# Kernel tuning notes

Measured on AMD Instinct MI355X. Metric: run time of the kernel, lower is better.

The kernel has to match this reference:

```python
import jax, jax.numpy as jnp
import numpy as np

N = 50000      # nodes
E = 1600000    # edges (avg degree 32)
F = 11         # atom_features
ED = 4         # edge_dim
L = 4          # num_layers
G = 500        # graphs in batch


def _lin(k, fi, fo, layers=True):
    s = 1.0 / np.sqrt(fi)
    kw, kb = jax.random.split(k)
    sw = (L, fi, fo) if layers else (fi, fo)
    sb = (L, fo) if layers else (fo,)
    return (jax.random.uniform(kw, sw, jnp.float32, -s, s),
            jax.random.uniform(kb, sb, jnp.float32, -s, s))


def setup_inputs() -> dict:
    key = jax.random.key(0)
    ks = jax.random.split(key, 16)
    inp = {}
    inp["h"] = jax.random.normal(ks[0], (N, F), jnp.float32)
    inp["pos"] = jax.random.normal(ks[1], (N, 3), jnp.float32)
    inp["edge_index"] = jax.random.randint(ks[2], (2, E), 0, N)
    inp["edge_attr"] = jax.random.normal(ks[3], (E, ED), jnp.float32)
    inp["batch"] = jnp.sort(jax.random.randint(ks[4], (N,), 0, G))
    # stacked per-layer linear params
    specs = [("W_msg1", "b_msg1", 2 * F + 1 + ED, F),
             ("W_msg2", "b_msg2", F, F),
             ("W_attn", "b_attn", F, 1),
             ("W_upd1", "b_upd1", 2 * F, F),
             ("W_upd2", "b_upd2", F, F),
             ("W_x1", "b_x1", 2 * F + 1 + ED, F),
             ("W_x2", "b_x2", F, F),
             ("W_x3", "b_x3", F, 1)]
    for i, (wn, bn, fi, fo) in enumerate(specs):
        w, b = _lin(ks[5 + i], fi, fo)
        inp[wn] = w
        inp[bn] = b
    w, b = _lin(ks[14], F, 1, layers=False)
    inp["W_pred"] = w
    inp["b_pred"] = b
    return inp


def reference(h, pos, edge_index, edge_attr, batch,
              W_msg1, b_msg1, W_msg2, b_msg2, W_attn, b_attn,
              W_upd1, b_upd1, W_upd2, b_upd2,
              W_x1, b_x1, W_x2, b_x2, W_x3, b_x3,
              W_pred, b_pred):
    src, dst = edge_index[0], edge_index[1]  # j (source), i (target)
    x = pos
    for l in range(L):
        h_i, h_j = h[dst], h[src]
        x_i, x_j = x[dst], x[src]
        d = jnp.linalg.norm(x_j - x_i, axis=-1, keepdims=True)  # [E,1]
        feat = jnp.concatenate([h_i, h_j, d * d, edge_attr], axis=-1)  # [E,27]
        m = jax.nn.silu(feat @ W_msg1[l] + b_msg1[l])
        m = jax.nn.silu(m @ W_msg2[l] + b_msg2[l])
        attn = jax.nn.sigmoid(m @ W_attn[l] + b_attn[l])
        msg_h = attn * m                                          # [E,F]
        phi = jax.nn.silu(feat @ W_x1[l] + b_x1[l])
        phi = jax.nn.silu(phi @ W_x2[l] + b_x2[l])
        phi = phi @ W_x3[l] + b_x3[l]                             # [E,1]
        msg_x = (x_i - x_j) / (d + 1.0) * phi                     # [E,3]
        agg_h = jax.ops.segment_sum(msg_h, dst, num_segments=N)
        agg_x = jax.ops.segment_sum(msg_x, dst, num_segments=N)
        upd = jax.nn.silu(jnp.concatenate([h, agg_h], axis=-1) @ W_upd1[l] + b_upd1[l])
        upd = upd @ W_upd2[l] + b_upd2[l]
        h = h + upd          # residual (h = h + h_upd in outer loop)
        x = x + agg_x        # out_x = x + agg_x
    # global mean pool over graphs, then linear head
    counts = jax.ops.segment_sum(jnp.ones((N, 1), h.dtype), batch, num_segments=G)
    h_graph = jax.ops.segment_sum(h, batch, num_segments=G) / jnp.maximum(counts, 1.0)
    return (h_graph @ W_pred + b_pred).reshape(-1)
```

## Files before the change

kernel.cpp:

```cpp
#include <hip/hip_runtime.h>

#define N_NODES 50000
#define N_EDGES 1600000
#define F 11
#define FEAT 27
#define NLAYERS 4
#define NGRAPH 500
#define NVALS 14
#define PRESTRIDE 24
#define NBLK 196

__device__ __forceinline__ float siluf(float v) { return v * (1.0f / (1.0f + __expf(-v))); }
__device__ __forceinline__ float sigmf(float v) { return 1.0f / (1.0f + __expf(-v)); }

__global__ __launch_bounds__(256) void hist_kernel(const int* __restrict__ dst,
                                                   int* __restrict__ deg) {
    int e = blockIdx.x * 256 + threadIdx.x;
    if (e < N_EDGES) atomicAdd(&deg[dst[e]], 1);
}

__global__ __launch_bounds__(256) void scan1_kernel(const int* __restrict__ deg,
                                                    int* __restrict__ part,
                                                    int* __restrict__ bsum) {
    int t = threadIdx.x;
    int i = blockIdx.x * 256 + t;
    int v = (i < N_NODES) ? deg[i] : 0;
    int lane = t & 63, wid = t >> 6;
    int s = v;
    #pragma unroll
    for (int off = 1; off < 64; off <<= 1) {
        int u = __shfl_up(s, off);
        if (lane >= off) s += u;
    }
    __shared__ int wsum[4];
    if (lane == 63) wsum[wid] = s;
    __syncthreads();
    int wpre = 0;
    #pragma unroll
    for (int w = 0; w < 4; ++w) if (w < wid) wpre += wsum[w];
    if (i < N_NODES) part[i] = s + wpre - v;
    if (t == 255) bsum[blockIdx.x] = s + wpre;
}

__global__ __launch_bounds__(256) void scan2_kernel(int* __restrict__ bsum) {
    int t = threadIdx.x;
    int v = (t < NBLK) ? bsum[t] : 0;
    int lane = t & 63, wid = t >> 6;
    int s = v;
    #pragma unroll
    for (int off = 1; off < 64; off <<= 1) {
        int u = __shfl_up(s, off);
        if (lane >= off) s += u;
    }
    __shared__ int wsum[4];
    if (lane == 63) wsum[wid] = s;
    __syncthreads();
    int wpre = 0;
    #pragma unroll
    for (int w = 0; w < 4; ++w) if (w < wid) wpre += wsum[w];
    if (t < NBLK) bsum[t] = s + wpre - v;
}

__global__ __launch_bounds__(256) void scan3_kernel(const int* __restrict__ part,
                                                    const int* __restrict__ bsum,
                                                    int* __restrict__ cursor) {
    int i = blockIdx.x * 256 + threadIdx.x;
    if (i < N_NODES) cursor[i] = part[i] + bsum[blockIdx.x];
}

__global__ __launch_bounds__(256) void scatter_kernel(
    const int* __restrict__ src, const int* __restrict__ dst,
    const float* __restrict__ eattr, int* __restrict__ cursor,
    int* __restrict__ ssrc, int* __restrict__ sdst, float4* __restrict__ sea) {
    int e = blockIdx.x * 256 + threadIdx.x;
    if (e >= N_EDGES) return;
    int d = dst[e];
    int pos = atomicAdd(&cursor[d], 1);
    ssrc[pos] = src[e];
    sdst[pos] = d;
    sea[pos] = reinterpret_cast<const float4*>(eattr)[e];
}

__global__ __launch_bounds__(256) void init_kernel(
    const float* __restrict__ h0, const float* __restrict__ pos,
    float* __restrict__ h, float* __restrict__ x,
    const float* __restrict__ Wm1, const float* __restrict__ bm1,
    const float* __restrict__ Wx1, const float* __restrict__ bx1,
    float* __restrict__ preA, float* __restrict__ preB)
{
    __shared__ float sM[2 * F * F], sX[2 * F * F], sbm[F], sbx[F];
    int t = threadIdx.x;
    for (int i2 = t; i2 < 2 * F * F; i2 += 256) { sM[i2] = Wm1[i2]; sX[i2] = Wx1[i2]; }
    if (t < F) { sbm[t] = bm1[t]; sbx[t] = bx1[t]; }
    __syncthreads();

    int n = blockIdx.x * 256 + t;
    if (n >= N_NODES) return;

    float hv[F];
    #pragma unroll
    for (int f2 = 0; f2 < F; ++f2) { hv[f2] = h0[n * F + f2]; h[n * F + f2] = hv[f2]; }
    #pragma unroll
    for (int k = 0; k < 3; ++k) x[n * 3 + k] = pos[n * 3 + k];

    float am[F], bm_[F], ax[F], bx_[F];
    #pragma unroll
    for (int o = 0; o < F; ++o) { am[o] = sbm[o]; ax[o] = sbx[o]; bm_[o] = 0.f; bx_[o] = 0.f; }
    #pragma unroll
    for (int fi = 0; fi < F; ++fi) {
        float v = hv[fi];
        #pragma unroll
        for (int o = 0; o < F; ++o) {
            am[o]  = fmaf(v, sM[fi * F + o], am[o]);
            bm_[o] = fmaf(v, sM[(F + fi) * F + o], bm_[o]);
            ax[o]  = fmaf(v, sX[fi * F + o], ax[o]);
            bx_[o] = fmaf(v, sX[(F + fi) * F + o], bx_[o]);
        }
    }
    #pragma unroll
    for (int o = 0; o < F; ++o) {
        preA[n * PRESTRIDE + o]     = am[o];
        preA[n * PRESTRIDE + F + o] = ax[o];
        preB[n * PRESTRIDE + o]     = bm_[o];
        preB[n * PRESTRIDE + F + o] = bx_[o];
    }
}

__global__ __launch_bounds__(256) void edge_kernel(
    const float* __restrict__ preA, const float* __restrict__ preB,
    const float* __restrict__ x,
    const int* __restrict__ ssrc, const int* __restrict__ sdst,
    const float4* __restrict__ sea,
    const float* __restrict__ Wm1,
    const float* __restrict__ Wm2, const float* __restrict__ bm2,
    const float* __restrict__ Wa,  const float* __restrict__ ba,
    const float* __restrict__ Wx1,
    const float* __restrict__ Wx2, const float* __restrict__ bx2,
    const float* __restrict__ Wx3, const float* __restrict__ bx3,
    float* __restrict__ agg_h, float* __restrict__ agg_x)
{
    __shared__ float sWm2[F * F], sWx2[F * F];
    __shared__ float sMd2[F], sMea[4 * F], sXd2[F], sXea[4 * F];
    __shared__ float sbm2[F], sWa[F], sbx2[F], sWx3[F];
    __shared__ float sba, sbx3;
    int t = threadIdx.x;
    for (int i2 = t; i2 < F * F; i2 += 256) { sWm2[i2] = Wm2[i2]; sWx2[i2] = Wx2[i2]; }
    if (t < F) {
        sMd2[t] = Wm1[22 * F + t]; sXd2[t] = Wx1[22 * F + t];
        sbm2[t] = bm2[t]; sWa[t] = Wa[t]; sbx2[t] = bx2[t]; sWx3[t] = Wx3[t];
    }
    if (t >= 64 && t < 64 + 4 * F) { int k = t - 64; sMea[k] = Wm1[23 * F + k]; sXea[k] = Wx1[23 * F + k]; }
    if (t == 0) { sba = ba[0]; sbx3 = bx3[0]; }
    __syncthreads();

    int e = blockIdx.x * 256 + t;
    if (e >= N_EDGES) return;

    int j = ssrc[e];
    int d = sdst[e];

    float pav[22], pbv[22];
    {
        const float4* pa4 = reinterpret_cast<const float4*>(preA + (size_t)d * PRESTRIDE);
        const float4* pb4 = reinterpret_cast<const float4*>(preB + (size_t)j * PRESTRIDE);
        #pragma unroll
        for (int q = 0; q < 5; ++q) {
            float4 va = pa4[q], vb = pb4[q];
            pav[4 * q + 0] = va.x; pav[4 * q + 1] = va.y; pav[4 * q + 2] = va.z; pav[4 * q + 3] = va.w;
            pbv[4 * q + 0] = vb.x; pbv[4 * q + 1] = vb.y; pbv[4 * q + 2] = vb.z; pbv[4 * q + 3] = vb.w;
        }
        float2 ta = *reinterpret_cast<const float2*>(preA + (size_t)d * PRESTRIDE + 20);
        float2 tb = *reinterpret_cast<const float2*>(preB + (size_t)j * PRESTRIDE + 20);
        pav[20] = ta.x; pav[21] = ta.y; pbv[20] = tb.x; pbv[21] = tb.y;
    }

    float xi0 = x[d * 3 + 0], xi1 = x[d * 3 + 1], xi2 = x[d * 3 + 2];
    float xj0 = x[j * 3 + 0], xj1 = x[j * 3 + 1], xj2 = x[j * 3 + 2];
    float dx = xj0 - xi0, dy = xj1 - xi1, dz = xj2 - xi2;
    float d2 = dx * dx + dy * dy + dz * dz;
    float4 ea = sea[e];

    float tm[F], tx[F];
    #pragma unroll
    for (int o = 0; o < F; ++o) {
        tm[o] = pav[o] + pbv[o];
        tx[o] = pav[F + o] + pbv[F + o];
    }
    #pragma unroll
    for (int o = 0; o < F; ++o) {
        tm[o] = fmaf(d2, sMd2[o], tm[o]);
        tx[o] = fmaf(d2, sXd2[o], tx[o]);
    }
    float eav[4] = {ea.x, ea.y, ea.z, ea.w};
    #pragma unroll
    for (int k = 0; k < 4; ++k) {
        float v = eav[k];
        #pragma unroll
        for (int o = 0; o < F; ++o) {
            tm[o] = fmaf(v, sMea[k * F + o], tm[o]);
            tx[o] = fmaf(v, sXea[k * F + o], tx[o]);
        }
    }
    #pragma unroll
    for (int o = 0; o < F; ++o) { tm[o] = siluf(tm[o]); tx[o] = siluf(tx[o]); }

    float m2[F], p2[F];
    #pragma unroll
    for (int o = 0; o < F; ++o) { m2[o] = sbm2[o]; p2[o] = sbx2[o]; }
    #pragma unroll
    for (int fi = 0; fi < F; ++fi) {
        float a = tm[fi], b = tx[fi];
        #pragma unroll
        for (int o = 0; o < F; ++o) {
            m2[o] = fmaf(a, sWm2[fi * F + o], m2[o]);
            p2[o] = fmaf(b, sWx2[fi * F + o], p2[o]);
        }
    }
    #pragma unroll
    for (int o = 0; o < F; ++o) { m2[o] = siluf(m2[o]); p2[o] = siluf(p2[o]); }

    float attn = sba, phi = sbx3;
    #pragma unroll
    for (int o = 0; o < F; ++o) {
        attn = fmaf(m2[o], sWa[o], attn);
        phi  = fmaf(p2[o], sWx3[o], phi);
    }
    attn = sigmf(attn);

    float dist = sqrtf(d2);
    float sc = phi / (dist + 1.0f);

    float vals[NVALS];
    #pragma unroll
    for (int o = 0; o < F; ++o) vals[o] = attn * m2[o];
    vals[F + 0] = (xi0 - xj0) * sc;
    vals[F + 1] = (xi1 - xj1) * sc;
    vals[F + 2] = (xi2 - xj2) * sc;

    int lane = t & 63;
    #pragma unroll
    for (int off = 1; off < 64; off <<= 1) {
        int du = __shfl_down(d, off);
        bool ok = (lane + off < 64) && (du == d);
        #pragma unroll
        for (int k = 0; k < NVALS; ++k) {
            float up = __shfl_down(vals[k], off);
            if (ok) vals[k] += up;
        }
    }
    int dprev = __shfl_up(d, 1);
    if (lane == 0 || dprev != d) {
        #pragma unroll
        for (int o = 0; o < F; ++o) unsafeAtomicAdd(&agg_h[d * F + o], vals[o]);
        unsafeAtomicAdd(&agg_x[d * 3 + 0], vals[F + 0]);
        unsafeAtomicAdd(&agg_x[d * 3 + 1], vals[F + 1]);
        unsafeAtomicAdd(&agg_x[d * 3 + 2], vals[F + 2]);
    }
}

__global__ __launch_bounds__(256) void node_kernel(
    float* __restrict__ h, float* __restrict__ x,
    const float* __restrict__ agg_h, const float* __restrict__ agg_x,
    const float* __restrict__ Wu1, const float* __restrict__ bu1,
    const float* __restrict__ Wu2, const float* __restrict__ bu2,
    const float* __restrict__ Wm1n, const float* __restrict__ bm1n,
    const float* __restrict__ Wx1n, const float* __restrict__ bx1n,
    float* __restrict__ preA, float* __restrict__ preB, int has_next)
{
    __shared__ float sWu1[2 * F * F], sWu2[F * F], sbu1[F], sbu2[F];
    __shared__ float sM[2 * F * F], sX[2 * F * F], sbm[F], sbx[F];
    int t = threadIdx.x;
    for (int i2 = t; i2 < 2 * F * F; i2 += 256) sWu1[i2] = Wu1[i2];
    for (int i2 = t; i2 < F * F; i2 += 256)     sWu2[i2] = Wu2[i2];
    if (t < F) { sbu1[t] = bu1[t]; sbu2[t] = bu2[t]; }
    if (has_next) {
        for (int i2 = t; i2 < 2 * F * F; i2 += 256) { sM[i2] = Wm1n[i2]; sX[i2] = Wx1n[i2]; }
        if (t < F) { sbm[t] = bm1n[t]; sbx[t] = bx1n[t]; }
    }
    __syncthreads();

    int n = blockIdx.x * 256 + t;
    if (n >= N_NODES) return;

    float in[2 * F];
    #pragma unroll
    for (int f2 = 0; f2 < F; ++f2) in[f2] = h[n * F + f2];
    #pragma unroll
    for (int f2 = 0; f2 < F; ++f2) in[F + f2] = agg_h[n * F + f2];

    float u[F];
    #pragma unroll
    for (int o = 0; o < F; ++o) u[o] = sbu1[o];
    #pragma unroll
    for (int fi = 0; fi < 2 * F; ++fi) {
        float fv = in[fi];
        #pragma unroll
        for (int o = 0; o < F; ++o) u[o] = fmaf(fv, sWu1[fi * F + o], u[o]);
    }
    #pragma unroll
    for (int o = 0; o < F; ++o) u[o] = siluf(u[o]);

    float hn[F];
    #pragma unroll
    for (int o = 0; o < F; ++o) hn[o] = in[o] + sbu2[o];
    #pragma unroll
    for (int fi = 0; fi < F; ++fi) {
        float fv = u[fi];
        #pragma unroll
        for (int o = 0; o < F; ++o) hn[o] = fmaf(fv, sWu2[fi * F + o], hn[o]);
    }

    #pragma unroll
    for (int f2 = 0; f2 < F; ++f2) h[n * F + f2] = hn[f2];
    #pragma unroll
    for (int k = 0; k < 3; ++k) x[n * 3 + k] += agg_x[n * 3 + k];

    if (has_next) {
        float am[F], bm_[F], ax[F], bx_[F];
        #pragma unroll
        for (int o = 0; o < F; ++o) { am[o] = sbm[o]; ax[o] = sbx[o]; bm_[o] = 0.f; bx_[o] = 0.f; }
        #pragma unroll
        for (int fi = 0; fi < F; ++fi) {
            float v = hn[fi];
            #pragma unroll
            for (int o = 0; o < F; ++o) {
                am[o]  = fmaf(v, sM[fi * F + o], am[o]);
                bm_[o] = fmaf(v, sM[(F + fi) * F + o], bm_[o]);
                ax[o]  = fmaf(v, sX[fi * F + o], ax[o]);
                bx_[o] = fmaf(v, sX[(F + fi) * F + o], bx_[o]);
            }
        }
        #pragma unroll
        for (int o = 0; o < F; ++o) {
            preA[n * PRESTRIDE + o]     = am[o];
            preA[n * PRESTRIDE + F + o] = ax[o];
            preB[n * PRESTRIDE + o]     = bm_[o];
            preB[n * PRESTRIDE + F + o] = bx_[o];
        }
    }
}

__global__ __launch_bounds__(256) void pool_kernel(
    const float* __restrict__ h, const int* __restrict__ batch,
    float* __restrict__ gsum, float* __restrict__ gcnt)
{
    int n = blockIdx.x * blockDim.x + threadIdx.x;
    int lane = threadIdx.x & 63;
    bool valid = (n < N_NODES);
    int g = valid ? batch[n] : -1;
    float vals[F + 1];
    #pragma unroll
    for (int f2 = 0; f2 < F; ++f2) vals[f2] = valid ? h[n * F + f2] : 0.0f;
    vals[F] = valid ? 1.0f : 0.0f;

    #pragma unroll
    for (int off = 1; off < 64; off <<= 1) {
        int gu = __shfl_down(g, off);
        bool ok = (lane + off < 64) && (gu == g);
        #pragma unroll
        for (int k = 0; k < F + 1; ++k) {
            float up = __shfl_down(vals[k], off);
            if (ok) vals[k] += up;
        }
    }
    int gprev = __shfl_up(g, 1);
    if (valid && (lane == 0 || gprev != g)) {
        #pragma unroll
        for (int f2 = 0; f2 < F; ++f2) unsafeAtomicAdd(&gsum[g * F + f2], vals[f2]);
        unsafeAtomicAdd(&gcnt[g], vals[F]);
    }
}

__global__ void head_kernel(const float* __restrict__ gsum, const float* __restrict__ gcnt,
                            const float* __restrict__ Wp, const float* __restrict__ bp,
                            float* __restrict__ out)
{
    int g = blockIdx.x * blockDim.x + threadIdx.x;
    if (g >= NGRAPH) return;
    float c = fmaxf(gcnt[g], 1.0f);
    float inv = 1.0f / c;
    float acc = bp[0];
    #pragma unroll
    for (int f2 = 0; f2 < F; ++f2) acc = fmaf(gsum[g * F + f2] * inv, Wp[f2], acc);
    out[g] = acc;
}

extern "C" void kernel_launch(void* const* d_in, const int* in_sizes, int n_in,
                              void* d_out, int out_size, void* d_ws, size_t ws_size,
                              hipStream_t stream)
{
    const float* h0    = (const float*)d_in[0];
    const float* pos   = (const float*)d_in[1];
    const int*   eidx  = (const int*)d_in[2];
    const float* eattr = (const float*)d_in[3];
    const int*   batch = (const int*)d_in[4];
    const float* Wm1 = (const float*)d_in[5];
    const float* bm1 = (const float*)d_in[6];
    const float* Wm2 = (const float*)d_in[7];
    const float* bm2 = (const float*)d_in[8];
    const float* Wa  = (const float*)d_in[9];
    const float* ba  = (const float*)d_in[10];
    const float* Wu1 = (const float*)d_in[11];
    const float* bu1 = (const float*)d_in[12];
    const float* Wu2 = (const float*)d_in[13];
    const float* bu2 = (const float*)d_in[14];
    const float* Wx1 = (const float*)d_in[15];
    const float* bx1 = (const float*)d_in[16];
    const float* Wx2 = (const float*)d_in[17];
    const float* bx2 = (const float*)d_in[18];
    const float* Wx3 = (const float*)d_in[19];
    const float* bx3 = (const float*)d_in[20];
    const float* Wp  = (const float*)d_in[21];
    const float* bp  = (const float*)d_in[22];

    char* base = (char*)d_ws;
    float4* sea  = (float4*)base;                         base += (size_t)N_EDGES * 16;
    float* preA  = (float*)base;                          base += (size_t)N_NODES * PRESTRIDE * 4;
    float* preB  = (float*)base;                          base += (size_t)N_NODES * PRESTRIDE * 4;
    float* h_cur = (float*)base;                          base += (size_t)N_NODES * F * 4;
    float* x_cur = (float*)base;                          base += (size_t)N_NODES * 3 * 4;
    float* agg_h = (float*)base;                          base += (size_t)N_NODES * F * 4;
    float* agg_x = (float*)base;                          base += (size_t)N_NODES * 3 * 4;
    float* gsum  = (float*)base;                          base += (size_t)NGRAPH * F * 4;
    float* gcnt  = (float*)base;                          base += (size_t)NGRAPH * 4;
    int*   deg   = (int*)base;                            base += (size_t)N_NODES * 4;
    int*   part  = (int*)base;                            base += (size_t)N_NODES * 4;
    int*   bsum  = (int*)base;                            base += (size_t)256 * 4;
    int*   cursor= (int*)base;                            base += (size_t)N_NODES * 4;
    int*   ssrc  = (int*)base;                            base += (size_t)N_EDGES * 4;
    int*   sdst  = (int*)base;                            base += (size_t)N_EDGES * 4;

    const int* src = eidx;
    const int* dst = eidx + N_EDGES;

    hipMemsetAsync(deg, 0, (size_t)N_NODES * sizeof(int), stream);
    hist_kernel<<<(N_EDGES + 255) / 256, 256, 0, stream>>>(dst, deg);
    scan1_kernel<<<NBLK, 256, 0, stream>>>(deg, part, bsum);
    scan2_kernel<<<1, 256, 0, stream>>>(bsum);
    scan3_kernel<<<NBLK, 256, 0, stream>>>(part, bsum, cursor);
    scatter_kernel<<<(N_EDGES + 255) / 256, 256, 0, stream>>>(
        src, dst, eattr, cursor, ssrc, sdst, sea);

    init_kernel<<<NBLK, 256, 0, stream>>>(h0, pos, h_cur, x_cur,
                                          Wm1, bm1, Wx1, bx1, preA, preB);

    for (int l = 0; l < NLAYERS; ++l) {
        hipMemsetAsync(agg_h, 0, (size_t)(N_NODES * (F + 3)) * sizeof(float), stream);
        edge_kernel<<<(N_EDGES + 255) / 256, 256, 0, stream>>>(
            preA, preB, x_cur, ssrc, sdst, sea,
            Wm1 + l * FEAT * F,
            Wm2 + l * F * F,    bm2 + l * F,
            Wa + l * F,         ba + l,
            Wx1 + l * FEAT * F,
            Wx2 + l * F * F,    bx2 + l * F,
            Wx3 + l * F,        bx3 + l,
            agg_h, agg_x);
        int nl = l + 1;
        int has_next = (nl < NLAYERS) ? 1 : 0;
        int wl = has_next ? nl : l;
        node_kernel<<<NBLK, 256, 0, stream>>>(
            h_cur, x_cur, agg_h, agg_x,
            Wu1 + l * 2 * F * F, bu1 + l * F,
            Wu2 + l * F * F,     bu2 + l * F,
            Wm1 + wl * FEAT * F, bm1 + wl * F,
            Wx1 + wl * FEAT * F, bx1 + wl * F,
            preA, preB, has_next);
    }

    hipMemsetAsync(gsum, 0, (size_t)(NGRAPH * F + NGRAPH) * sizeof(float), stream);
    pool_kernel<<<(N_NODES + 255) / 256, 256, 0, stream>>>(h_cur, batch, gsum, gcnt);
    head_kernel<<<2, 256, 0, stream>>>(gsum, gcnt, Wp, bp, (float*)d_out);
}
```

Before: 684.1 us.

## Pad edge MLP to 12 lanes with packed FMA and split CSR scatter into perm+gather

The edge MLP now pads the 11-wide hidden vectors to 12 and computes them with v_pk_fma_f32 two lanes at a time. Weights sit in shared memory as float4 and the node precompute rows use an aligned 12+12 layout with zeroed padding. The CSR build now scatters only a permutation index and then gathers src, dst and edge attributes in a separate coalesced pass. This targets VALU instruction count in the edge kernel and the scattered multi-array writes in the scatter, at the cost of one extra kernel and buffer plus inline asm.

```diff
diff --git a/kernel.cpp b/kernel.cpp
--- a/kernel.cpp
+++ b/kernel.cpp
@@ -13,6 +13,17 @@
 __device__ __forceinline__ float siluf(float v) { return v * (1.0f / (1.0f + __expf(-v))); }
 __device__ __forceinline__ float sigmf(float v) { return 1.0f / (1.0f + __expf(-v)); }
 
+__device__ __forceinline__ float2 pkfma(float2 a, float2 b, float2 c) {
+    float2 d;
+    asm("v_pk_fma_f32 %0, %1, %2, %3" : "=v"(d) : "v"(a), "v"(b), "v"(c));
+    return d;
+}
+__device__ __forceinline__ void rank1_pk(float v, const float4 w, float2& a0, float2& a1) {
+    float2 vv = make_float2(v, v);
+    a0 = pkfma(vv, make_float2(w.x, w.y), a0);
+    a1 = pkfma(vv, make_float2(w.z, w.w), a1);
+}
+
 __global__ __launch_bounds__(256) void hist_kernel(const int* __restrict__ dst,
                                                    int* __restrict__ deg) {
     int e = blockIdx.x * 256 + threadIdx.x;
@@ -68,17 +79,26 @@
     if (i < N_NODES) cursor[i] = part[i] + bsum[blockIdx.x];
 }
 
-__global__ __launch_bounds__(256) void scatter_kernel(
-    const int* __restrict__ src, const int* __restrict__ dst,
-    const float* __restrict__ eattr, int* __restrict__ cursor,
-    int* __restrict__ ssrc, int* __restrict__ sdst, float4* __restrict__ sea) {
+__global__ __launch_bounds__(256) void scatter_perm(const int* __restrict__ dst,
+                                                    int* __restrict__ cursor,
+                                                    int* __restrict__ perm) {
     int e = blockIdx.x * 256 + threadIdx.x;
     if (e >= N_EDGES) return;
     int d = dst[e];
     int pos = atomicAdd(&cursor[d], 1);
-    ssrc[pos] = src[e];
-    sdst[pos] = d;
-    sea[pos] = reinterpret_cast<const float4*>(eattr)[e];
+    perm[pos] = e;
+}
+
+__global__ __launch_bounds__(256) void mat_kernel(
+    const int* __restrict__ perm, const int* __restrict__ src,
+    const int* __restrict__ dst, const float4* __restrict__ eattr4,
+    int* __restrict__ ssrc, int* __restrict__ sdst, float4* __restrict__ sea) {
+    int i = blockIdx.x * 256 + threadIdx.x;
+    if (i >= N_EDGES) return;
+    int e = perm[i];
+    ssrc[i] = src[e];
+    sdst[i] = dst[e];
+    sea[i] = eattr4[e];
 }
 
 __global__ __launch_bounds__(256) void init_kernel(
@@ -119,11 +139,13 @@
     }
     #pragma unroll
     for (int o = 0; o < F; ++o) {
-        preA[n * PRESTRIDE + o]     = am[o];
-        preA[n * PRESTRIDE + F + o] = ax[o];
-        preB[n * PRESTRIDE + o]     = bm_[o];
-        preB[n * PRESTRIDE + F + o] = bx_[o];
-    }
+        preA[n * PRESTRIDE + o]      = am[o];
+        preA[n * PRESTRIDE + 12 + o] = ax[o];
+        preB[n * PRESTRIDE + o]      = bm_[o];
+        preB[n * PRESTRIDE + 12 + o] = bx_[o];
+    }
+    preA[n * PRESTRIDE + 11] = 0.f; preA[n * PRESTRIDE + 23] = 0.f;
+    preB[n * PRESTRIDE + 11] = 0.f; preB[n * PRESTRIDE + 23] = 0.f;
 }
 
 __global__ __launch_bounds__(256) void edge_kernel(
@@ -139,18 +161,34 @@
     const float* __restrict__ Wx3, const float* __restrict__ bx3,
     float* __restrict__ agg_h, float* __restrict__ agg_x)
 {
-    __shared__ float sWm2[F * F], sWx2[F * F];
-    __shared__ float sMd2[F], sMea[4 * F], sXd2[F], sXea[4 * F];
-    __shared__ float sbm2[F], sWa[F], sbx2[F], sWx3[F];
+    __shared__ float4 sW2m[F * 3], sW2x[F * 3];
+    __shared__ float4 sD2m[3], sD2x[3], sEAm[4 * 3], sEAx[4 * 3];
+    __shared__ float4 sB2m[3], sB2x[3], sWav[3], sWx3v[3];
     __shared__ float sba, sbx3;
     int t = threadIdx.x;
-    for (int i2 = t; i2 < F * F; i2 += 256) { sWm2[i2] = Wm2[i2]; sWx2[i2] = Wx2[i2]; }
-    if (t < F) {
-        sMd2[t] = Wm1[22 * F + t]; sXd2[t] = Wx1[22 * F + t];
-        sbm2[t] = bm2[t]; sWa[t] = Wa[t]; sbx2[t] = bx2[t]; sWx3[t] = Wx3[t];
-    }
-    if (t >= 64 && t < 64 + 4 * F) { int k = t - 64; sMea[k] = Wm1[23 * F + k]; sXea[k] = Wx1[23 * F + k]; }
-    if (t == 0) { sba = ba[0]; sbx3 = bx3[0]; }
+    {
+        float* w2m = (float*)sW2m; float* w2x = (float*)sW2x;
+        for (int i2 = t; i2 < F * 12; i2 += 256) {
+            int r = i2 / 12, c = i2 % 12;
+            w2m[i2] = (c < F) ? Wm2[r * F + c] : 0.f;
+            w2x[i2] = (c < F) ? Wx2[r * F + c] : 0.f;
+        }
+        float* eam = (float*)sEAm; float* eax = (float*)sEAx;
+        for (int i2 = t; i2 < 4 * 12; i2 += 256) {
+            int r = i2 / 12, c = i2 % 12;
+            eam[i2] = (c < F) ? Wm1[(23 + r) * F + c] : 0.f;
+            eax[i2] = (c < F) ? Wx1[(23 + r) * F + c] : 0.f;
+        }
+        if (t < 12) {
+            ((float*)sD2m)[t] = (t < F) ? Wm1[22 * F + t] : 0.f;
+            ((float*)sD2x)[t] = (t < F) ? Wx1[22 * F + t] : 0.f;
+            ((float*)sB2m)[t] = (t < F) ? bm2[t] : 0.f;
+            ((float*)sB2x)[t] = (t < F) ? bx2[t] : 0.f;
+            ((float*)sWav)[t] = (t < F) ? Wa[t] : 0.f;
+            ((float*)sWx3v)[t] = (t < F) ? Wx3[t] : 0.f;
+        }
+        if (t == 0) { sba = ba[0]; sbx3 = bx3[0]; }
+    }
     __syncthreads();
 
     int e = blockIdx.x * 256 + t;
@@ -159,19 +197,12 @@
     int j = ssrc[e];
     int d = sdst[e];
 
-    float pav[22], pbv[22];
+    float4 pa[6], pb[6];
     {
         const float4* pa4 = reinterpret_cast<const float4*>(preA + (size_t)d * PRESTRIDE);
         const float4* pb4 = reinterpret_cast<const float4*>(preB + (size_t)j * PRESTRIDE);
         #pragma unroll
-        for (int q = 0; q < 5; ++q) {
-            float4 va = pa4[q], vb = pb4[q];
-            pav[4 * q + 0] = va.x; pav[4 * q + 1] = va.y; pav[4 * q + 2] = va.z; pav[4 * q + 3] = va.w;
-            pbv[4 * q + 0] = vb.x; pbv[4 * q + 1] = vb.y; pbv[4 * q + 2] = vb.z; pbv[4 * q + 3] = vb.w;
-        }
-        float2 ta = *reinterpret_cast<const float2*>(preA + (size_t)d * PRESTRIDE + 20);
-        float2 tb = *reinterpret_cast<const float2*>(preB + (size_t)j * PRESTRIDE + 20);
-        pav[20] = ta.x; pav[21] = ta.y; pbv[20] = tb.x; pbv[21] = tb.y;
+        for (int q = 0; q < 6; ++q) { pa[q] = pa4[q]; pb[q] = pb4[q]; }
     }
 
     float xi0 = x[d * 3 + 0], xi1 = x[d * 3 + 1], xi2 = x[d * 3 + 2];
@@ -180,59 +211,88 @@
     float d2 = dx * dx + dy * dy + dz * dz;
     float4 ea = sea[e];
 
-    float tm[F], tx[F];
-    #pragma unroll
-    for (int o = 0; o < F; ++o) {
-        tm[o] = pav[o] + pbv[o];
-        tx[o] = pav[F + o] + pbv[F + o];
-    }
-    #pragma unroll
-    for (int o = 0; o < F; ++o) {
-        tm[o] = fmaf(d2, sMd2[o], tm[o]);
-        tx[o] = fmaf(d2, sXd2[o], tx[o]);
+    float2 am[6], axv[6];
+    #pragma unroll
+    for (int q = 0; q < 3; ++q) {
+        float4 sm, sx;
+        sm.x = pa[q].x + pb[q].x; sm.y = pa[q].y + pb[q].y;
+        sm.z = pa[q].z + pb[q].z; sm.w = pa[q].w + pb[q].w;
+        sx.x = pa[3 + q].x + pb[3 + q].x; sx.y = pa[3 + q].y + pb[3 + q].y;
+        sx.z = pa[3 + q].z + pb[3 + q].z; sx.w = pa[3 + q].w + pb[3 + q].w;
+        am[2 * q]     = make_float2(sm.x, sm.y);
+        am[2 * q + 1] = make_float2(sm.z, sm.w);
+        axv[2 * q]     = make_float2(sx.x, sx.y);
+        axv[2 * q + 1] = make_float2(sx.z, sx.w);
+    }
+    #pragma unroll
+    for (int qq = 0; qq < 3; ++qq) {
+        rank1_pk(d2, sD2m[qq], am[2 * qq], am[2 * qq + 1]);
+        rank1_pk(d2, sD2x[qq], axv[2 * qq], axv[2 * qq + 1]);
     }
     float eav[4] = {ea.x, ea.y, ea.z, ea.w};
     #pragma unroll
     for (int k = 0; k < 4; ++k) {
-        float v = eav[k];
-        #pragma unroll
-        for (int o = 0; o < F; ++o) {
-            tm[o] = fmaf(v, sMea[k * F + o], tm[o]);
-            tx[o] = fmaf(v, sXea[k * F + o], tx[o]);
-        }
+        #pragma unroll
+        for (int qq = 0; qq < 3; ++qq) {
+            rank1_pk(eav[k], sEAm[k * 3 + qq], am[2 * qq], am[2 * qq + 1]);
+            rank1_pk(eav[k], sEAx[k * 3 + qq], axv[2 * qq], axv[2 * qq + 1]);
+        }
+    }
+
+    float tm[12], tx[12];
+    #pragma unroll
+    for (int q = 0; q < 6; ++q) {
+        tm[2 * q] = am[q].x; tm[2 * q + 1] = am[q].y;
+        tx[2 * q] = axv[q].x; tx[2 * q + 1] = axv[q].y;
     }
     #pragma unroll
     for (int o = 0; o < F; ++o) { tm[o] = siluf(tm[o]); tx[o] = siluf(tx[o]); }
 
-    float m2[F], p2[F];
-    #pragma unroll
-    for (int o = 0; o < F; ++o) { m2[o] = sbm2[o]; p2[o] = sbx2[o]; }
+    float2 m2a[6], p2a[6];
+    {
+        const float2* b2m = (const float2*)sB2m;
+        const float2* b2x = (const float2*)sB2x;
+        #pragma unroll
+        for (int q = 0; q < 6; ++q) { m2a[q] = b2m[q]; p2a[q] = b2x[q]; }
+    }
     #pragma unroll
     for (int fi = 0; fi < F; ++fi) {
         float a = tm[fi], b = tx[fi];
         #pragma unroll
-        for (int o = 0; o < F; ++o) {
-            m2[o] = fmaf(a, sWm2[fi * F + o], m2[o]);
-            p2[o] = fmaf(b, sWx2[fi * F + o], p2[o]);
-        }
-    }
-    #pragma unroll
-    for (int o = 0; o < F; ++o) { m2[o] = siluf(m2[o]); p2[o] = siluf(p2[o]); }
-
-    float attn = sba, phi = sbx3;
-    #pragma unroll
-    for (int o = 0; o < F; ++o) {
-        attn = fmaf(m2[o], sWa[o], attn);
-        phi  = fmaf(p2[o], sWx3[o], phi);
-    }
-    attn = sigmf(attn);
+        for (int qq = 0; qq < 3; ++qq) {
+            rank1_pk(a, sW2m[fi * 3 + qq], m2a[2 * qq], m2a[2 * qq + 1]);
+            rank1_pk(b, sW2x[fi * 3 + qq], p2a[2 * qq], p2a[2 * qq + 1]);
+        }
+    }
+    float m2s[12], p2s[12];
+    #pragma unroll
+    for (int q = 0; q < 6; ++q) {
+        m2s[2 * q] = m2a[q].x; m2s[2 * q + 1] = m2a[q].y;
+        p2s[2 * q] = p2a[q].x; p2s[2 * q + 1] = p2a[q].y;
+    }
+    #pragma unroll
+    for (int o = 0; o < F; ++o) { m2s[o] = siluf(m2s[o]); p2s[o] = siluf(p2s[o]); }
+    m2s[11] = 0.f; p2s[11] = 0.f;
+
+    float2 accA = make_float2(0.f, 0.f), accP = make_float2(0.f, 0.f);
+    {
+        const float2* wa = (const float2*)sWav;
+        const float2* w3 = (const float2*)sWx3v;
+        #pragma unroll
+        for (int q = 0; q < 6; ++q) {
+            accA = pkfma(make_float2(m2s[2 * q], m2s[2 * q + 1]), wa[q], accA);
+            accP = pkfma(make_float2(p2s[2 * q], p2s[2 * q + 1]), w3[q], accP);
+        }
+    }
+    float attn = sigmf(sba + accA.x + accA.y);
+    float phi  = sbx3 + accP.x + accP.y;
 
     float dist = sqrtf(d2);
     float sc = phi / (dist + 1.0f);
 
     float vals[NVALS];
     #pragma unroll
-    for (int o = 0; o < F; ++o) vals[o] = attn * m2[o];
+    for (int o = 0; o < F; ++o) vals[o] = attn * m2s[o];
     vals[F + 0] = (xi0 - xj0) * sc;
     vals[F + 1] = (xi1 - xj1) * sc;
     vals[F + 2] = (xi2 - xj2) * sc;
@@ -332,11 +392,13 @@
         }
         #pragma unroll
         for (int o = 0; o < F; ++o) {
-            preA[n * PRESTRIDE + o]     = am[o];
-            preA[n * PRESTRIDE + F + o] = ax[o];
-            preB[n * PRESTRIDE + o]     = bm_[o];
-            preB[n * PRESTRIDE + F + o] = bx_[o];
-        }
+            preA[n * PRESTRIDE + o]      = am[o];
+            preA[n * PRESTRIDE + 12 + o] = ax[o];
+            preB[n * PRESTRIDE + o]      = bm_[o];
+            preB[n * PRESTRIDE + 12 + o] = bx_[o];
+        }
+        preA[n * PRESTRIDE + 11] = 0.f; preA[n * PRESTRIDE + 23] = 0.f;
+        preB[n * PRESTRIDE + 11] = 0.f; preB[n * PRESTRIDE + 23] = 0.f;
     }
 }
 
@@ -427,6 +489,7 @@
     int*   part  = (int*)base;                            base += (size_t)N_NODES * 4;
     int*   bsum  = (int*)base;                            base += (size_t)256 * 4;
     int*   cursor= (int*)base;                            base += (size_t)N_NODES * 4;
+    int*   perm  = (int*)base;                            base += (size_t)N_EDGES * 4;
     int*   ssrc  = (int*)base;                            base += (size_t)N_EDGES * 4;
     int*   sdst  = (int*)base;                            base += (size_t)N_EDGES * 4;
 
@@ -438,8 +501,9 @@
     scan1_kernel<<<NBLK, 256, 0, stream>>>(deg, part, bsum);
     scan2_kernel<<<1, 256, 0, stream>>>(bsum);
     scan3_kernel<<<NBLK, 256, 0, stream>>>(part, bsum, cursor);
-    scatter_kernel<<<(N_EDGES + 255) / 256, 256, 0, stream>>>(
-        src, dst, eattr, cursor, ssrc, sdst, sea);
+    scatter_perm<<<(N_EDGES + 255) / 256, 256, 0, stream>>>(dst, cursor, perm);
+    mat_kernel<<<(N_EDGES + 255) / 256, 256, 0, stream>>>(
+        perm, src, dst, reinterpret_cast<const float4*>(eattr), ssrc, sdst, sea);
 
     init_kernel<<<NBLK, 256, 0, stream>>>(h0, pos, h_cur, x_cur,
                                           Wm1, bm1, Wx1, bx1, preA, preB);
```

Result: slower. 807.0 us (+18.0%).
